# Kernel tuning notes

Hardware: AMD Instinct MI355X
Metric: run time of the kernel (lower is better)

## Reference

```python
import jax, jax.numpy as jnp
import numpy as np

N_NODES = 100000
N_EDGES = 3200000
D_FEAT = 512
HIDDEN = 16
N_CLASSES = 7


def setup_inputs() -> dict:
    key = jax.random.key(0)
    k1, k2, k3, k4 = jax.random.split(key, 4)
    x = jax.random.normal(k1, (N_NODES, D_FEAT), dtype=jnp.float32)
    edge_index = jax.random.randint(k2, (2, N_EDGES), 0, N_NODES, dtype=jnp.int64)
    # Glorot-ish scaled weights
    W1 = jax.random.normal(k3, (D_FEAT, HIDDEN), dtype=jnp.float32) * (1.0 / np.sqrt(D_FEAT))
    b1 = jnp.zeros((HIDDEN,), dtype=jnp.float32)
    W2 = jax.random.normal(k4, (HIDDEN, N_CLASSES), dtype=jnp.float32) * (1.0 / np.sqrt(HIDDEN))
    b2 = jnp.zeros((N_CLASSES,), dtype=jnp.float32)
    return {"x": x, "edge_index": edge_index, "W1": W1, "b1": b1, "W2": W2, "b2": b2}


def _gcn_norm(edge_index, num_nodes):
    # Add self-loops, then symmetric normalization: D^-1/2 A D^-1/2
    loop = jnp.arange(num_nodes, dtype=edge_index.dtype)
    src = jnp.concatenate([edge_index[0], loop])
    dst = jnp.concatenate([edge_index[1], loop])
    deg = jax.ops.segment_sum(jnp.ones_like(dst, dtype=jnp.float32), dst,
                              num_segments=num_nodes)
    dinv = jnp.where(deg > 0, jax.lax.rsqrt(deg), 0.0)
    w = dinv[src] * dinv[dst]  # [E+N]
    return src, dst, w


def _gcn_conv(x, W, b, src, dst, w, num_nodes):
    h = x @ W                               # transform first (small out dim)
    m = jax.ops.segment_sum(h[src] * w[:, None], dst, num_segments=num_nodes)
    return m + b


def reference(x, edge_index, W1, b1, W2, b2):
    n = x.shape[0]
    src, dst, w = _gcn_norm(edge_index, n)
    h = jax.nn.relu(_gcn_conv(x, W1, b1, src, dst, w, n))
    # dropout is identity at inference
    logits = _gcn_conv(h, W2, b2, src, dst, w, n)
    return jax.nn.log_softmax(logits, axis=1)
```

## Files before the change

kernel.cpp:

```cpp
#include <hip/hip_runtime.h>
#include <cmath>

#define N_NODES   100000
#define N_EDGES   3200000
#define D_FEAT    512
#define HIDDEN    16
#define N_CLASSES 7

#define NCHUNK 250
#define CHUNK  12800
#define NBKT   1563

typedef __attribute__((ext_vector_type(4))) float  f32x4;
typedef __attribute__((ext_vector_type(8))) short  bf16x8;

__device__ __forceinline__ short f2bf(float f) {
    union { float f; unsigned u; } v; v.f = f;
    unsigned r = v.u + 0x7fffu + ((v.u >> 16) & 1u);
    return (short)(r >> 16);
}
__device__ __forceinline__ float bf2f(unsigned short s) {
    union { unsigned u; float f; } v; v.u = ((unsigned)s) << 16;
    return v.f;
}

__global__ __launch_bounds__(256) void k_zero(unsigned* __restrict__ p, int n) {
    int i = blockIdx.x * 256 + threadIdx.x;
    if (i < n) p[i] = 0u;
}

__global__ __launch_bounds__(1024) void k_hist(const int* __restrict__ dst,
                                               unsigned* __restrict__ bucket_count) {
    __shared__ unsigned h[NBKT];
    int t = threadIdx.x, b = blockIdx.x;
    for (int i = t; i < NBKT; i += 1024) h[i] = 0u;
    __syncthreads();
    int base = b * CHUNK;
    #pragma unroll 2
    for (int k = 0; k < 13; ++k) {
        int idx = k * 1024 + t;
        if (idx < CHUNK) atomicAdd(&h[((unsigned)dst[base + idx]) >> 6], 1u);
    }
    __syncthreads();
    for (int i = t; i < NBKT; i += 1024) {
        unsigned v = h[i];
        if (v) atomicAdd(&bucket_count[i], v);
    }
}

__global__ __launch_bounds__(256) void k_scan(const unsigned* __restrict__ bucket_count,
                                              unsigned* __restrict__ bin_base,
                                              unsigned* __restrict__ bin_cursor) {
    __shared__ unsigned t0[256];
    int t = threadIdx.x;
    unsigned running = 0u;
    for (int c0 = 0; c0 < NBKT; c0 += 256) {
        int i = c0 + t;
        unsigned v = (i < NBKT) ? bucket_count[i] : 0u;
        t0[t] = v; __syncthreads();
        #pragma unroll
        for (int off = 1; off < 256; off <<= 1) {
            unsigned add = (t >= off) ? t0[t - off] : 0u;
            __syncthreads();
            t0[t] += add;
            __syncthreads();
        }
        if (i < NBKT) {
            unsigned e = running + t0[t] - v;
            bin_base[i]   = e;
            bin_cursor[i] = e;
        }
        unsigned chunk_sum = t0[255];
        __syncthreads();
        running += chunk_sum;
    }
    if (t == 0) bin_base[NBKT] = running;
}

__global__ __launch_bounds__(1024) void k_scatter(const int* __restrict__ src,
                                                  const int* __restrict__ dst,
                                                  unsigned* __restrict__ bin_cursor,
                                                  unsigned* __restrict__ packed) {
    __shared__ unsigned h[NBKT];
    int t = threadIdx.x, b = blockIdx.x;
    for (int i = t; i < NBKT; i += 1024) h[i] = 0u;
    __syncthreads();
    int base = b * CHUNK;
    #pragma unroll 2
    for (int k = 0; k < 13; ++k) {
        int idx = k * 1024 + t;
        if (idx < CHUNK) atomicAdd(&h[((unsigned)dst[base + idx]) >> 6], 1u);
    }
    __syncthreads();
    for (int i = t; i < NBKT; i += 1024) {
        unsigned c = h[i];
        h[i] = c ? atomicAdd(&bin_cursor[i], c) : 0u;
    }
    __syncthreads();
    #pragma unroll 2
    for (int k = 0; k < 13; ++k) {
        int idx = k * 1024 + t;
        if (idx < CHUNK) {
            int e = base + idx;
            unsigned d = (unsigned)dst[e];
            unsigned pos = atomicAdd(&h[d >> 6], 1u);
            packed[pos] = ((d & 63u) << 24) | (unsigned)src[e];
        }
    }
}

__global__ __launch_bounds__(256) void k_bucket(const unsigned* __restrict__ packed,
                                                const unsigned* __restrict__ bin_base,
                                                unsigned* __restrict__ deg,
                                                unsigned* __restrict__ row_start,
                                                float* __restrict__ dinv,
                                                int* __restrict__ csr_src) {
    __shared__ unsigned hh[4][64], sc[64], cur[64];
    int t = threadIdx.x, b = blockIdx.x;
    int w = t >> 6, l = t & 63;
    unsigned rs = bin_base[b];
    unsigned re = bin_base[b + 1];
    hh[w][l] = 0u;
    __syncthreads();
    for (unsigned i = rs + t; i < re; i += 256)
        atomicAdd(&hh[w][packed[i] >> 24], 1u);
    __syncthreads();
    unsigned total = 0u;
    if (t < 64) {
        total = hh[0][t] + hh[1][t] + hh[2][t] + hh[3][t];
        sc[t] = total;
    }
    __syncthreads();
    #pragma unroll
    for (int off = 1; off < 64; off <<= 1) {
        unsigned add = (t >= off && t < 64) ? sc[t - off] : 0u;
        __syncthreads();
        if (t < 64) sc[t] += add;
        __syncthreads();
    }
    if (t < 64) {
        unsigned excl = sc[t] - total;
        int node = b * 64 + t;
        if (node < N_NODES) {
            deg[node]       = total;
            row_start[node] = rs + excl;
            dinv[node]      = rsqrtf((float)(total + 1u));
        }
        cur[t] = rs + excl;
    }
    __syncthreads();
    for (unsigned i = rs + t; i < re; i += 256) {
        unsigned p = packed[i];
        unsigned pos = atomicAdd(&cur[p >> 24], 1u);
        csr_src[pos] = (int)(p & 0xFFFFFFu);
    }
}

__global__ __launch_bounds__(256) void k_gemm1(const float* __restrict__ x,
                                               const float* __restrict__ w1,
                                               const float* __restrict__ dinv,
                                               unsigned short* __restrict__ h1p) {
    __shared__ __align__(16) short w1t[16][520];
    int tid = threadIdx.x;
    for (int idx = tid; idx < D_FEAT * HIDDEN; idx += 256) {
        int k = idx >> 4, n = idx & 15;
        w1t[n][k] = f2bf(w1[idx]);
    }
    __syncthreads();

    int lane = tid & 63, wid = tid >> 6;
    int m  = lane & 15;
    int kg = lane >> 4;

    bf16x8 bfrag[16];
    #pragma unroll
    for (int ks = 0; ks < 16; ++ks)
        bfrag[ks] = *(const bf16x8*)&w1t[m][ks * 32 + kg * 8];

    int tile = blockIdx.x * 4 + wid;
    if (tile >= (N_NODES / 16)) return;

    const f32x4* xr = (const f32x4*)(x + (size_t)(tile * 16 + m) * D_FEAT);
    f32x4 acc = {0.f, 0.f, 0.f, 0.f};
    #pragma unroll
    for (int ks = 0; ks < 16; ++ks) {
        f32x4 x0 = xr[ks * 8 + kg * 2];
        f32x4 x1 = xr[ks * 8 + kg * 2 + 1];
        bf16x8 a;
        a[0] = f2bf(x0[0]); a[1] = f2bf(x0[1]); a[2] = f2bf(x0[2]); a[3] = f2bf(x0[3]);
        a[4] = f2bf(x1[0]); a[5] = f2bf(x1[1]); a[6] = f2bf(x1[2]); a[7] = f2bf(x1[3]);
        acc = __builtin_amdgcn_mfma_f32_16x16x32_bf16(a, bfrag[ks], acc, 0, 0, 0);
    }
    size_t base = (size_t)tile * 256;
    #pragma unroll
    for (int r = 0; r < 4; ++r) {
        int rr = kg * 4 + r;
        h1p[base + rr * 16 + m] = (unsigned short)f2bf(dinv[tile * 16 + rr] * acc[r]);
    }
}

__global__ __launch_bounds__(256) void k_gather1(const int* __restrict__ csr_src,
                                                 const unsigned* __restrict__ row_start,
                                                 const unsigned* __restrict__ deg,
                                                 const unsigned short* __restrict__ h1p,
                                                 const float* __restrict__ dinv,
                                                 const float* __restrict__ w2,
                                                 const float* __restrict__ b1,
                                                 float* __restrict__ h2p) {
    __shared__ float w2s[16][8];
    __shared__ float b1s[16];
    int tid  = threadIdx.x;
    if (tid < 128) {
        int jj = tid >> 3, c = tid & 7;
        w2s[jj][c] = (c < N_CLASSES) ? w2[jj * N_CLASSES + c] : 0.f;
    }
    if (tid < 16) b1s[tid] = b1[tid];
    __syncthreads();

    int lane = tid & 63;
    int node = blockIdx.x * 4 + (tid >> 6);
    int j  = lane & 15;
    int sl = lane >> 4;

    unsigned start = row_start[node];
    unsigned end   = start + deg[node];

    float acc = (sl == 0) ? bf2f(h1p[(size_t)node * 16 + j]) : 0.f;
    unsigned e = start;
    for (; e + 16 <= end; e += 16) {
        int s0 = csr_src[e      + sl];
        int s1 = csr_src[e + 4  + sl];
        int s2 = csr_src[e + 8  + sl];
        int s3 = csr_src[e + 12 + sl];
        float v0 = bf2f(h1p[(size_t)s0 * 16 + j]);
        float v1 = bf2f(h1p[(size_t)s1 * 16 + j]);
        float v2 = bf2f(h1p[(size_t)s2 * 16 + j]);
        float v3 = bf2f(h1p[(size_t)s3 * 16 + j]);
        acc += v0; acc += v1; acc += v2; acc += v3;
    }
    for (; e < end; e += 4) {
        unsigned idx = e + (unsigned)sl;
        float v = 0.f;
        if (idx < end) v = bf2f(h1p[(size_t)csr_src[idx] * 16 + j]);
        acc += v;
    }
    acc += __shfl_down(acc, 32);
    acc += __shfl_down(acc, 16);

    float di = dinv[node];
    float hv = fmaxf(fmaf(di, acc, b1s[j]), 0.f);
    float o = 0.f;
    int c = lane & 7;
    #pragma unroll
    for (int jj = 0; jj < 16; ++jj)
        o = fmaf(__shfl(hv, jj), w2s[jj][c], o);
    if (lane < 8)
        h2p[(size_t)node * 8 + c] = (c < N_CLASSES) ? di * o : 0.f;
}

__global__ __launch_bounds__(256) void k_gather2(const int* __restrict__ csr_src,
                                                 const unsigned* __restrict__ row_start,
                                                 const unsigned* __restrict__ deg,
                                                 const float* __restrict__ dinv,
                                                 const float* __restrict__ h2p,
                                                 const float* __restrict__ b2,
                                                 float* __restrict__ out) {
    int tid  = threadIdx.x;
    int lane = tid & 63;
    int node = blockIdx.x * 4 + (tid >> 6);
    int j  = lane & 7;
    int sl = lane >> 3;

    unsigned start = row_start[node];
    unsigned end   = start + deg[node];

    float acc = (sl == 0) ? h2p[(size_t)node * 8 + j] : 0.f;
    unsigned e = start;
    for (; e + 32 <= end; e += 32) {
        int s0 = csr_src[e      + sl];
        int s1 = csr_src[e + 8  + sl];
        int s2 = csr_src[e + 16 + sl];
        int s3 = csr_src[e + 24 + sl];
        float v0 = h2p[(size_t)s0 * 8 + j];
        float v1 = h2p[(size_t)s1 * 8 + j];
        float v2 = h2p[(size_t)s2 * 8 + j];
        float v3 = h2p[(size_t)s3 * 8 + j];
        acc += v0; acc += v1; acc += v2; acc += v3;
    }
    for (; e < end; e += 8) {
        unsigned idx = e + (unsigned)sl;
        float v = 0.f;
        if (idx < end) v = h2p[(size_t)csr_src[idx] * 8 + j];
        acc += v;
    }
    acc += __shfl_down(acc, 32);
    acc += __shfl_down(acc, 16);
    acc += __shfl_down(acc, 8);
    float di = dinv[node];
    float logit = (j < N_CLASSES) ? di * acc + b2[j] : -1e30f;
    float mx = logit;
    #pragma unroll
    for (int mk = 1; mk < 8; mk <<= 1) mx = fmaxf(mx, __shfl_xor(mx, mk, 8));
    float ex = (j < N_CLASSES) ? __expf(logit - mx) : 0.f;
    float sum = ex;
    #pragma unroll
    for (int mk = 1; mk < 8; mk <<= 1) sum += __shfl_xor(sum, mk, 8);
    if (sl == 0 && j < N_CLASSES)
        out[(size_t)node * N_CLASSES + j] = logit - mx - __logf(sum);
}

extern "C" void kernel_launch(void* const* d_in, const int* in_sizes, int n_in,
                              void* d_out, int out_size, void* d_ws, size_t ws_size,
                              hipStream_t stream) {
    const float* x  = (const float*)d_in[0];
    const int*   ei = (const int*)d_in[1];
    const float* w1 = (const float*)d_in[2];
    const float* b1 = (const float*)d_in[3];
    const float* w2 = (const float*)d_in[4];
    const float* b2 = (const float*)d_in[5];
    float* out = (float*)d_out;

    const int* src = ei;
    const int* dst = ei + N_EDGES;

    unsigned* w32            = (unsigned*)d_ws;
    float*    dinv           = (float*)(w32 + 0);
    unsigned short* h1p      = (unsigned short*)(w32 + 102400);
    float*    h2p            = (float*)(w32 + 902400);
    unsigned* deg            = w32 + 1702400;
    unsigned* row_start      = w32 + 1804800;
    unsigned* bucket_count   = w32 + 1907200;
    unsigned* bin_base       = w32 + 1909248;
    unsigned* bin_cursor     = w32 + 1911296;
    unsigned* packed         = w32 + 1913344;
    int*      csr_src        = (int*)(w32 + 5113344);

    const int GB = (N_NODES / 16 + 3) / 4;

    k_zero    <<<(NBKT + 255) / 256, 256, 0, stream>>>(bucket_count, NBKT);
    k_hist    <<<NCHUNK, 1024, 0, stream>>>(dst, bucket_count);
    k_scan    <<<1,      256,  0, stream>>>(bucket_count, bin_base, bin_cursor);
    k_scatter <<<NCHUNK, 1024, 0, stream>>>(src, dst, bin_cursor, packed);
    k_bucket  <<<NBKT,   256,  0, stream>>>(packed, bin_base, deg, row_start, dinv, csr_src);
    k_gemm1   <<<GB,     256,  0, stream>>>(x, w1, dinv, h1p);
    k_gather1 <<<25000,  256,  0, stream>>>(csr_src, row_start, deg, h1p, dinv, w2, b1, h2p);
    k_gather2 <<<25000,  256,  0, stream>>>(csr_src, row_start, deg, dinv, h2p, b2, out);
}
```

Before: 497.4 us.

## Drop full CSR build; aggregate per 64-node bucket with LDS atomics

Removes the second-level per-node sort into CSR (row_start, deg, csr_src) and instead has both aggregation kernels process the bucket-sorted packed edge list directly. Each block owns one 64-node bucket and accumulates neighbor features into shared memory with atomicAdd before applying the epilogue (ReLU+W2 or log-softmax). A small degree-only kernel replaces the bucket kernel, and the zeroing kernel becomes a memset. This saves the CSR write and the scan, at the cost of LDS atomic contention and reduced per-node parallelism in the epilogue.

```diff
diff --git a/kernel.cpp b/kernel.cpp
--- a/kernel.cpp
+++ b/kernel.cpp
@@ -22,11 +22,6 @@
 __device__ __forceinline__ float bf2f(unsigned short s) {
     union { unsigned u; float f; } v; v.u = ((unsigned)s) << 16;
     return v.f;
-}
-
-__global__ __launch_bounds__(256) void k_zero(unsigned* __restrict__ p, int n) {
-    int i = blockIdx.x * 256 + threadIdx.x;
-    if (i < n) p[i] = 0u;
 }
 
 __global__ __launch_bounds__(1024) void k_hist(const int* __restrict__ dst,
@@ -109,50 +104,24 @@
     }
 }
 
-__global__ __launch_bounds__(256) void k_bucket(const unsigned* __restrict__ packed,
-                                                const unsigned* __restrict__ bin_base,
-                                                unsigned* __restrict__ deg,
-                                                unsigned* __restrict__ row_start,
-                                                float* __restrict__ dinv,
-                                                int* __restrict__ csr_src) {
-    __shared__ unsigned hh[4][64], sc[64], cur[64];
+__global__ __launch_bounds__(256) void k_deg(const unsigned* __restrict__ packed,
+                                             const unsigned* __restrict__ bin_base,
+                                             float* __restrict__ dinv) {
+    __shared__ unsigned hh[4][64];
     int t = threadIdx.x, b = blockIdx.x;
     int w = t >> 6, l = t & 63;
-    unsigned rs = bin_base[b];
-    unsigned re = bin_base[b + 1];
+    unsigned rs = bin_base[b], re = bin_base[b + 1];
     hh[w][l] = 0u;
     __syncthreads();
     for (unsigned i = rs + t; i < re; i += 256)
         atomicAdd(&hh[w][packed[i] >> 24], 1u);
     __syncthreads();
-    unsigned total = 0u;
     if (t < 64) {
-        total = hh[0][t] + hh[1][t] + hh[2][t] + hh[3][t];
-        sc[t] = total;
-    }
-    __syncthreads();
-    #pragma unroll
-    for (int off = 1; off < 64; off <<= 1) {
-        unsigned add = (t >= off && t < 64) ? sc[t - off] : 0u;
-        __syncthreads();
-        if (t < 64) sc[t] += add;
-        __syncthreads();
-    }
-    if (t < 64) {
-        unsigned excl = sc[t] - total;
         int node = b * 64 + t;
         if (node < N_NODES) {
-            deg[node]       = total;
-            row_start[node] = rs + excl;
-            dinv[node]      = rsqrtf((float)(total + 1u));
-        }
-        cur[t] = rs + excl;
-    }
-    __syncthreads();
-    for (unsigned i = rs + t; i < re; i += 256) {
-        unsigned p = packed[i];
-        unsigned pos = atomicAdd(&cur[p >> 24], 1u);
-        csr_src[pos] = (int)(p & 0xFFFFFFu);
+            unsigned total = hh[0][t] + hh[1][t] + hh[2][t] + hh[3][t];
+            dinv[node] = rsqrtf((float)(total + 1u));
+        }
     }
 }
 
@@ -199,114 +168,109 @@
     }
 }
 
-__global__ __launch_bounds__(256) void k_gather1(const int* __restrict__ csr_src,
-                                                 const unsigned* __restrict__ row_start,
-                                                 const unsigned* __restrict__ deg,
+__global__ __launch_bounds__(256) void k_gatherA(const unsigned* __restrict__ packed,
+                                                 const unsigned* __restrict__ bin_base,
                                                  const unsigned short* __restrict__ h1p,
                                                  const float* __restrict__ dinv,
                                                  const float* __restrict__ w2,
                                                  const float* __restrict__ b1,
                                                  float* __restrict__ h2p) {
+    __shared__ float acc[64][17];
     __shared__ float w2s[16][8];
     __shared__ float b1s[16];
-    int tid  = threadIdx.x;
-    if (tid < 128) {
-        int jj = tid >> 3, c = tid & 7;
-        w2s[jj][c] = (c < N_CLASSES) ? w2[jj * N_CLASSES + c] : 0.f;
-    }
-    if (tid < 16) b1s[tid] = b1[tid];
-    __syncthreads();
-
-    int lane = tid & 63;
-    int node = blockIdx.x * 4 + (tid >> 6);
-    int j  = lane & 15;
-    int sl = lane >> 4;
-
-    unsigned start = row_start[node];
-    unsigned end   = start + deg[node];
-
-    float acc = (sl == 0) ? bf2f(h1p[(size_t)node * 16 + j]) : 0.f;
-    unsigned e = start;
-    for (; e + 16 <= end; e += 16) {
-        int s0 = csr_src[e      + sl];
-        int s1 = csr_src[e + 4  + sl];
-        int s2 = csr_src[e + 8  + sl];
-        int s3 = csr_src[e + 12 + sl];
-        float v0 = bf2f(h1p[(size_t)s0 * 16 + j]);
-        float v1 = bf2f(h1p[(size_t)s1 * 16 + j]);
-        float v2 = bf2f(h1p[(size_t)s2 * 16 + j]);
-        float v3 = bf2f(h1p[(size_t)s3 * 16 + j]);
-        acc += v0; acc += v1; acc += v2; acc += v3;
-    }
-    for (; e < end; e += 4) {
-        unsigned idx = e + (unsigned)sl;
-        float v = 0.f;
-        if (idx < end) v = bf2f(h1p[(size_t)csr_src[idx] * 16 + j]);
-        acc += v;
-    }
-    acc += __shfl_down(acc, 32);
-    acc += __shfl_down(acc, 16);
-
-    float di = dinv[node];
-    float hv = fmaxf(fmaf(di, acc, b1s[j]), 0.f);
-    float o = 0.f;
-    int c = lane & 7;
-    #pragma unroll
-    for (int jj = 0; jj < 16; ++jj)
-        o = fmaf(__shfl(hv, jj), w2s[jj][c], o);
-    if (lane < 8)
-        h2p[(size_t)node * 8 + c] = (c < N_CLASSES) ? di * o : 0.f;
-}
-
-__global__ __launch_bounds__(256) void k_gather2(const int* __restrict__ csr_src,
-                                                 const unsigned* __restrict__ row_start,
-                                                 const unsigned* __restrict__ deg,
+    int t = threadIdx.x, b = blockIdx.x;
+    if (t < 128) { int jj = t >> 3, c = t & 7;
+                   w2s[jj][c] = (c < N_CLASSES) ? w2[jj * N_CLASSES + c] : 0.f; }
+    if (t < 16) b1s[t] = b1[t];
+    #pragma unroll
+    for (int k = 0; k < 4; ++k) {
+        int e = t + k * 256;
+        int l = e >> 4, j = e & 15;
+        int node = b * 64 + l;
+        acc[l][j] = (node < N_NODES) ? bf2f(h1p[(size_t)node * 16 + j]) : 0.f;
+    }
+    unsigned rs = bin_base[b], re = bin_base[b + 1];
+    __syncthreads();
+    int slot = t >> 4, j = t & 15;
+    #pragma unroll 2
+    for (unsigned i0 = rs; i0 < re; i0 += 16) {
+        unsigned idx = i0 + (unsigned)slot;
+        if (idx < re) {
+            unsigned p = packed[idx];
+            float v = bf2f(h1p[(size_t)(p & 0xFFFFFFu) * 16 + j]);
+            atomicAdd(&acc[p >> 24][j], v);
+        }
+    }
+    __syncthreads();
+    if (t < 64) {
+        int node = b * 64 + t;
+        if (node < N_NODES) {
+            float di = dinv[node];
+            float h[16];
+            #pragma unroll
+            for (int jj = 0; jj < 16; ++jj)
+                h[jj] = fmaxf(fmaf(di, acc[t][jj], b1s[jj]), 0.f);
+            float* h2r = h2p + (size_t)node * 8;
+            #pragma unroll
+            for (int c = 0; c < N_CLASSES; ++c) {
+                float o = 0.f;
+                #pragma unroll
+                for (int jj = 0; jj < 16; ++jj) o = fmaf(h[jj], w2s[jj][c], o);
+                h2r[c] = di * o;
+            }
+            h2r[7] = 0.f;
+        }
+    }
+}
+
+__global__ __launch_bounds__(256) void k_gatherB(const unsigned* __restrict__ packed,
+                                                 const unsigned* __restrict__ bin_base,
+                                                 const float* __restrict__ h2p,
                                                  const float* __restrict__ dinv,
-                                                 const float* __restrict__ h2p,
                                                  const float* __restrict__ b2,
                                                  float* __restrict__ out) {
-    int tid  = threadIdx.x;
-    int lane = tid & 63;
-    int node = blockIdx.x * 4 + (tid >> 6);
-    int j  = lane & 7;
-    int sl = lane >> 3;
-
-    unsigned start = row_start[node];
-    unsigned end   = start + deg[node];
-
-    float acc = (sl == 0) ? h2p[(size_t)node * 8 + j] : 0.f;
-    unsigned e = start;
-    for (; e + 32 <= end; e += 32) {
-        int s0 = csr_src[e      + sl];
-        int s1 = csr_src[e + 8  + sl];
-        int s2 = csr_src[e + 16 + sl];
-        int s3 = csr_src[e + 24 + sl];
-        float v0 = h2p[(size_t)s0 * 8 + j];
-        float v1 = h2p[(size_t)s1 * 8 + j];
-        float v2 = h2p[(size_t)s2 * 8 + j];
-        float v3 = h2p[(size_t)s3 * 8 + j];
-        acc += v0; acc += v1; acc += v2; acc += v3;
-    }
-    for (; e < end; e += 8) {
-        unsigned idx = e + (unsigned)sl;
-        float v = 0.f;
-        if (idx < end) v = h2p[(size_t)csr_src[idx] * 8 + j];
-        acc += v;
-    }
-    acc += __shfl_down(acc, 32);
-    acc += __shfl_down(acc, 16);
-    acc += __shfl_down(acc, 8);
-    float di = dinv[node];
-    float logit = (j < N_CLASSES) ? di * acc + b2[j] : -1e30f;
-    float mx = logit;
-    #pragma unroll
-    for (int mk = 1; mk < 8; mk <<= 1) mx = fmaxf(mx, __shfl_xor(mx, mk, 8));
-    float ex = (j < N_CLASSES) ? __expf(logit - mx) : 0.f;
-    float sum = ex;
-    #pragma unroll
-    for (int mk = 1; mk < 8; mk <<= 1) sum += __shfl_xor(sum, mk, 8);
-    if (sl == 0 && j < N_CLASSES)
-        out[(size_t)node * N_CLASSES + j] = logit - mx - __logf(sum);
+    __shared__ float acc[64][9];
+    int t = threadIdx.x, b = blockIdx.x;
+    #pragma unroll
+    for (int k = 0; k < 2; ++k) {
+        int e = t + k * 256;
+        int l = e >> 3, c = e & 7;
+        int node = b * 64 + l;
+        acc[l][c] = (node < N_NODES) ? h2p[(size_t)node * 8 + c] : 0.f;
+    }
+    unsigned rs = bin_base[b], re = bin_base[b + 1];
+    __syncthreads();
+    int slot = t >> 3, c = t & 7;
+    #pragma unroll 2
+    for (unsigned i0 = rs; i0 < re; i0 += 32) {
+        unsigned idx = i0 + (unsigned)slot;
+        if (idx < re) {
+            unsigned p = packed[idx];
+            float v = h2p[(size_t)(p & 0xFFFFFFu) * 8 + c];
+            atomicAdd(&acc[p >> 24][c], v);
+        }
+    }
+    __syncthreads();
+    if (t < 64) {
+        int node = b * 64 + t;
+        if (node < N_NODES) {
+            float di = dinv[node];
+            float lg[N_CLASSES];
+            float mx = -1e30f;
+            #pragma unroll
+            for (int cc = 0; cc < N_CLASSES; ++cc) {
+                lg[cc] = fmaf(di, acc[t][cc], b2[cc]);
+                mx = fmaxf(mx, lg[cc]);
+            }
+            float sum = 0.f;
+            #pragma unroll
+            for (int cc = 0; cc < N_CLASSES; ++cc) sum += __expf(lg[cc] - mx);
+            float lse = mx + __logf(sum);
+            float* orow = out + (size_t)node * N_CLASSES;
+            #pragma unroll
+            for (int cc = 0; cc < N_CLASSES; ++cc) orow[cc] = lg[cc] - lse;
+        }
+    }
 }
 
 extern "C" void kernel_launch(void* const* d_in, const int* in_sizes, int n_in,
@@ -327,22 +291,19 @@
     float*    dinv           = (float*)(w32 + 0);
     unsigned short* h1p      = (unsigned short*)(w32 + 102400);
     float*    h2p            = (float*)(w32 + 902400);
-    unsigned* deg            = w32 + 1702400;
-    unsigned* row_start      = w32 + 1804800;
-    unsigned* bucket_count   = w32 + 1907200;
-    unsigned* bin_base       = w32 + 1909248;
-    unsigned* bin_cursor     = w32 + 1911296;
-    unsigned* packed         = w32 + 1913344;
-    int*      csr_src        = (int*)(w32 + 5113344);
+    unsigned* bucket_count   = w32 + 1702400;
+    unsigned* bin_base       = w32 + 1704448;
+    unsigned* bin_cursor     = w32 + 1706496;
+    unsigned* packed         = w32 + 1708544;
 
     const int GB = (N_NODES / 16 + 3) / 4;
 
-    k_zero    <<<(NBKT + 255) / 256, 256, 0, stream>>>(bucket_count, NBKT);
+    hipMemsetAsync(bucket_count, 0, NBKT * sizeof(unsigned), stream);
     k_hist    <<<NCHUNK, 1024, 0, stream>>>(dst, bucket_count);
     k_scan    <<<1,      256,  0, stream>>>(bucket_count, bin_base, bin_cursor);
     k_scatter <<<NCHUNK, 1024, 0, stream>>>(src, dst, bin_cursor, packed);
-    k_bucket  <<<NBKT,   256,  0, stream>>>(packed, bin_base, deg, row_start, dinv, csr_src);
+    k_deg     <<<NBKT,   256,  0, stream>>>(packed, bin_base, dinv);
     k_gemm1   <<<GB,     256,  0, stream>>>(x, w1, dinv, h1p);
-    k_gather1 <<<25000,  256,  0, stream>>>(csr_src, row_start, deg, h1p, dinv, w2, b1, h2p);
-    k_gather2 <<<25000,  256,  0, stream>>>(csr_src, row_start, deg, dinv, h2p, b2, out);
-}
+    k_gatherA <<<NBKT,   256,  0, stream>>>(packed, bin_base, h1p, dinv, w2, b1, h2p);
+    k_gatherB <<<NBKT,   256,  0, stream>>>(packed, bin_base, h2p, dinv, b2, out);
+}
```

After: 837.3 us. +68.3%, slower.

## Replace histogram-scan-scatter with fixed-capacity bucket slots

Applied to the files above, without the earlier changes.

Removes the separate histogram pass, the single-block prefix scan and the zero kernel. Each destination bucket now gets a fixed slot of BCAP entries, so the scatter kernel claims positions with one global atomic per bucket. This saves a full extra read of the dst array and two kernel launches. The cost is a larger packed/csr buffer, plus silent overflow if any bucket receives more than BCAP edges; that holds for uniform random graphs but not for skewed ones.

```diff
diff --git a/kernel.cpp b/kernel.cpp
--- a/kernel.cpp
+++ b/kernel.cpp
@@ -10,6 +10,7 @@
 #define NCHUNK 250
 #define CHUNK  12800
 #define NBKT   1563
+#define BCAP   2560
 
 typedef __attribute__((ext_vector_type(4))) float  f32x4;
 typedef __attribute__((ext_vector_type(8))) short  bf16x8;
@@ -24,13 +25,10 @@
     return v.f;
 }
 
-__global__ __launch_bounds__(256) void k_zero(unsigned* __restrict__ p, int n) {
-    int i = blockIdx.x * 256 + threadIdx.x;
-    if (i < n) p[i] = 0u;
-}
-
-__global__ __launch_bounds__(1024) void k_hist(const int* __restrict__ dst,
-                                               unsigned* __restrict__ bucket_count) {
+__global__ __launch_bounds__(1024) void k_scatterD(const int* __restrict__ src,
+                                                   const int* __restrict__ dst,
+                                                   unsigned* __restrict__ cnt,
+                                                   unsigned* __restrict__ packed) {
     __shared__ unsigned h[NBKT];
     int t = threadIdx.x, b = blockIdx.x;
     for (int i = t; i < NBKT; i += 1024) h[i] = 0u;
@@ -43,58 +41,8 @@
     }
     __syncthreads();
     for (int i = t; i < NBKT; i += 1024) {
-        unsigned v = h[i];
-        if (v) atomicAdd(&bucket_count[i], v);
-    }
-}
-
-__global__ __launch_bounds__(256) void k_scan(const unsigned* __restrict__ bucket_count,
-                                              unsigned* __restrict__ bin_base,
-                                              unsigned* __restrict__ bin_cursor) {
-    __shared__ unsigned t0[256];
-    int t = threadIdx.x;
-    unsigned running = 0u;
-    for (int c0 = 0; c0 < NBKT; c0 += 256) {
-        int i = c0 + t;
-        unsigned v = (i < NBKT) ? bucket_count[i] : 0u;
-        t0[t] = v; __syncthreads();
-        #pragma unroll
-        for (int off = 1; off < 256; off <<= 1) {
-            unsigned add = (t >= off) ? t0[t - off] : 0u;
-            __syncthreads();
-            t0[t] += add;
-            __syncthreads();
-        }
-        if (i < NBKT) {
-            unsigned e = running + t0[t] - v;
-            bin_base[i]   = e;
-            bin_cursor[i] = e;
-        }
-        unsigned chunk_sum = t0[255];
-        __syncthreads();
-        running += chunk_sum;
-    }
-    if (t == 0) bin_base[NBKT] = running;
-}
-
-__global__ __launch_bounds__(1024) void k_scatter(const int* __restrict__ src,
-                                                  const int* __restrict__ dst,
-                                                  unsigned* __restrict__ bin_cursor,
-                                                  unsigned* __restrict__ packed) {
-    __shared__ unsigned h[NBKT];
-    int t = threadIdx.x, b = blockIdx.x;
-    for (int i = t; i < NBKT; i += 1024) h[i] = 0u;
-    __syncthreads();
-    int base = b * CHUNK;
-    #pragma unroll 2
-    for (int k = 0; k < 13; ++k) {
-        int idx = k * 1024 + t;
-        if (idx < CHUNK) atomicAdd(&h[((unsigned)dst[base + idx]) >> 6], 1u);
-    }
-    __syncthreads();
-    for (int i = t; i < NBKT; i += 1024) {
         unsigned c = h[i];
-        h[i] = c ? atomicAdd(&bin_cursor[i], c) : 0u;
+        h[i] = c ? ((unsigned)i * BCAP + atomicAdd(&cnt[i], c)) : 0u;
     }
     __syncthreads();
     #pragma unroll 2
@@ -110,7 +58,7 @@
 }
 
 __global__ __launch_bounds__(256) void k_bucket(const unsigned* __restrict__ packed,
-                                                const unsigned* __restrict__ bin_base,
+                                                const unsigned* __restrict__ cnt,
                                                 unsigned* __restrict__ deg,
                                                 unsigned* __restrict__ row_start,
                                                 float* __restrict__ dinv,
@@ -118,8 +66,8 @@
     __shared__ unsigned hh[4][64], sc[64], cur[64];
     int t = threadIdx.x, b = blockIdx.x;
     int w = t >> 6, l = t & 63;
-    unsigned rs = bin_base[b];
-    unsigned re = bin_base[b + 1];
+    unsigned rs = (unsigned)b * BCAP;
+    unsigned re = rs + cnt[b];
     hh[w][l] = 0u;
     __syncthreads();
     for (unsigned i = rs + t; i < re; i += 256)
@@ -329,19 +277,15 @@
     float*    h2p            = (float*)(w32 + 902400);
     unsigned* deg            = w32 + 1702400;
     unsigned* row_start      = w32 + 1804800;
-    unsigned* bucket_count   = w32 + 1907200;
-    unsigned* bin_base       = w32 + 1909248;
-    unsigned* bin_cursor     = w32 + 1911296;
-    unsigned* packed         = w32 + 1913344;
-    int*      csr_src        = (int*)(w32 + 5113344);
+    unsigned* cnt            = w32 + 1907200;
+    unsigned* packed         = w32 + 1909248;
+    int*      csr_src        = (int*)(w32 + 5910528);
 
     const int GB = (N_NODES / 16 + 3) / 4;
 
-    k_zero    <<<(NBKT + 255) / 256, 256, 0, stream>>>(bucket_count, NBKT);
-    k_hist    <<<NCHUNK, 1024, 0, stream>>>(dst, bucket_count);
-    k_scan    <<<1,      256,  0, stream>>>(bucket_count, bin_base, bin_cursor);
-    k_scatter <<<NCHUNK, 1024, 0, stream>>>(src, dst, bin_cursor, packed);
-    k_bucket  <<<NBKT,   256,  0, stream>>>(packed, bin_base, deg, row_start, dinv, csr_src);
+    hipMemsetAsync(cnt, 0, NBKT * sizeof(unsigned), stream);
+    k_scatterD<<<NCHUNK, 1024, 0, stream>>>(src, dst, cnt, packed);
+    k_bucket  <<<NBKT,   256,  0, stream>>>(packed, cnt, deg, row_start, dinv, csr_src);
     k_gemm1   <<<GB,     256,  0, stream>>>(x, w1, dinv, h1p);
     k_gather1 <<<25000,  256,  0, stream>>>(csr_src, row_start, deg, h1p, dinv, w2, b1, h2p);
     k_gather2 <<<25000,  256,  0, stream>>>(csr_src, row_start, deg, dinv, h2p, b2, out);
```

After: 487.4 us. 2.0% less time.
